# Optimization experiments

Measured on AMD Instinct MI355X. Metric: run time of the kernel, lower is better.

The kernel has to match this reference:

```python
import jax, jax.numpy as jnp
import numpy as np


def _conv1x1(w, b, x):
    # 1x1 Conv2d == channel matmul: w [O,C], x [B,C,H,W] -> [B,O,H,W]
    return jnp.einsum('oc,bchw->bohw', w, x) + b[None, :, None, None]


def setup_inputs() -> dict:
    key = jax.random.key(0)
    ks = jax.random.split(key, 9)
    C = 512
    B, H, W = 8, 32, 32
    s = 0.02
    return {
        'x': jax.random.normal(ks[0], (B, C, H, W), dtype=jnp.float32),
        'wq': jax.random.normal(ks[1], (C, C), dtype=jnp.float32) * s,
        'bq': jax.random.normal(ks[2], (C,), dtype=jnp.float32) * s,
        'wk': jax.random.normal(ks[3], (C, C), dtype=jnp.float32) * s,
        'bk': jax.random.normal(ks[4], (C,), dtype=jnp.float32) * s,
        'wv': jax.random.normal(ks[5], (C, C), dtype=jnp.float32) * s,
        'bv': jax.random.normal(ks[6], (C,), dtype=jnp.float32) * s,
        'wo': jax.random.normal(ks[7], (C, C), dtype=jnp.float32) * s,
        'bo': jax.random.normal(ks[8], (C,), dtype=jnp.float32) * s,
        'heads': 8,
    }


def reference(x, wq, bq, wk, bk, wv, bv, wo, bo, heads):
    B, C, H, W = x.shape
    N = H * W
    d = C // heads
    scale = jnp.asarray(d, x.dtype) ** 0.5

    vx = _conv1x1(wv, bv, x)                       # value(x), reused for residual
    Q = _conv1x1(wq, bq, x).reshape(B, heads, d, N)
    K = _conv1x1(wk, bk, x).reshape(B, heads, d, N)
    V = vx.reshape(B, heads, d, N)

    attn = jax.nn.softmax(jnp.einsum('bhcn,bhcm->bhnm', Q, K) / scale, axis=-1)
    attn_out = jnp.einsum('bhnm,bhcm->bhcn', attn, V).reshape(B, C, H, W)

    out = attn_out + vx                            # residual uses value(x)
    return _conv1x1(wo, bo, out)
```

## Files before the change

kernel.cpp:

```cpp
#include <hip/hip_runtime.h>
#include <cstdint>
#include <cmath>

#define B_ 8
#define C_ 512
#define N_ 1024
#define H_ 8
#define D_ 64


using u16 = unsigned short;

typedef __bf16 bf16x8 __attribute__((ext_vector_type(8)));
typedef float  f32x4  __attribute__((ext_vector_type(4)));
typedef unsigned short us8 __attribute__((ext_vector_type(8)));

#if __has_builtin(__builtin_amdgcn_exp2f)
#define EXP2(x) __builtin_amdgcn_exp2f(x)
#else
#define EXP2(x) exp2f(x)
#endif

#define QSCALE 0.1803368801111244f


__device__ __forceinline__ float b2f(u16 u) {
    return __uint_as_float(((uint32_t)u) << 16);
}
__device__ __forceinline__ u16 f2b(float f) {
    uint32_t x = __float_as_uint(f);
    return (u16)((x + 0x7fffu + ((x >> 16) & 1u)) >> 16);
}
__device__ __forceinline__ u16 f2bt(float f) {
    return (u16)(__float_as_uint(f) >> 16);
}
__device__ __forceinline__ float sf(float f) {
    return (fabsf(f) < 1e30f) ? f : 0.0f;
}
__device__ __forceinline__ u16 sf2b(float f) { return f2b(sf(f)); }

template<bool WB>
__device__ __forceinline__ us8 ldw(const void* W, size_t idx) {
    if constexpr (WB) {
        return *(const us8*)((const u16*)W + idx);
    } else {
        const float* p = (const float*)W + idx;
        float4 a = *(const float4*)p, b = *(const float4*)(p + 4);
        us8 pk;
        pk[0] = sf2b(a.x); pk[1] = sf2b(a.y); pk[2] = sf2b(a.z); pk[3] = sf2b(a.w);
        pk[4] = sf2b(b.x); pk[5] = sf2b(b.y); pk[6] = sf2b(b.z); pk[7] = sf2b(b.w);
        return pk;
    }
}


__global__ __launch_bounds__(256) void k_pre(const float* __restrict__ x,
                                             u16* __restrict__ xt,
                                             const float* __restrict__ wq,
                                             const float* __restrict__ wk,
                                             const float* __restrict__ wv,
                                             const float* __restrict__ wo,
                                             u16* __restrict__ wb) {
    const int tid = threadIdx.x;
    const int nb = blockIdx.x, cb = blockIdx.y, b = blockIdx.z;
    if (b == 8) {
        if (wb == nullptr) return;
        int base = (cb * 16 + nb) * 256 + tid;
#pragma unroll
        for (int i = 0; i < 8; ++i) {
            int idx = base + i * 32768;
            int m = idx >> 16;
            int off = (idx & 65535) << 2;
            const float* src = (m == 0) ? wq : (m == 1) ? wk : (m == 2) ? wv : wo;
            float4 v = *(const float4*)&src[off];
            ushort4 w;
            w.x = sf2b(v.x); w.y = sf2b(v.y); w.z = sf2b(v.z); w.w = sf2b(v.w);
            *(ushort4*)&wb[(m << 18) + off] = w;
        }
        return;
    }
    __shared__ __align__(16) u16 t[64][72];
#pragma unroll
    for (int i = 0; i < 4; ++i) {
        int q = tid + i * 256;
        int row = q >> 4, cg = q & 15;
        float4 v = *(const float4*)&x[((size_t)(b * C_ + cb * 64 + row) << 10) + nb * 64 + cg * 4];
        ushort4 w;
        w.x = sf2b(v.x); w.y = sf2b(v.y); w.z = sf2b(v.z); w.w = sf2b(v.w);
        *(ushort4*)&t[row][cg * 4] = w;
    }
    __syncthreads();
#pragma unroll
    for (int i = 0; i < 4; ++i) {
        int q = tid + i * 256;
        int nrow = q >> 4, cg = q & 15;
        ushort4 w;
        w.x = t[cg * 4 + 0][nrow];
        w.y = t[cg * 4 + 1][nrow];
        w.z = t[cg * 4 + 2][nrow];
        w.w = t[cg * 4 + 3][nrow];
        *(ushort4*)&xt[((size_t)(b * N_ + nb * 64 + nrow) << 9) + cb * 64 + cg * 4] = w;
    }
}


template<bool WB>
__global__ __launch_bounds__(256) void k_proj_t(
    const u16* __restrict__ xt,
    const void* __restrict__ wq, const float* __restrict__ bq,
    const void* __restrict__ wk, const float* __restrict__ bk,
    const void* __restrict__ wv, const float* __restrict__ bv,
    u16* __restrict__ qt, u16* __restrict__ kt,
    u16* __restrict__ v,  u16* __restrict__ vxt) {
    __shared__ __align__(16) u16 lA[128 * 64];
    __shared__ __align__(16) u16 lB[128 * 64];
    const int tid = threadIdx.x;
    const int op = blockIdx.z >> 3, b = blockIdx.z & 7;
    const int n0 = blockIdx.x * 128, o0 = blockIdx.y * 128;
    const void*  W  = (op == 0) ? wq : (op == 1) ? wk : wv;
    const float* BI = (op == 0) ? bq : (op == 1) ? bk : bv;
    const u16* A = xt + ((size_t)b << 19);
    const int lane = tid & 63, wave = tid >> 6;
    const int wm = (wave >> 1) * 64, wn = (wave & 1) * 64;
    const int l15 = lane & 15, lg = lane >> 4;
    const int xs = (l15 & 7) << 3;

    f32x4 acc[4][4];
    const f32x4 vzero = {0.f, 0.f, 0.f, 0.f};
#pragma unroll
    for (int i = 0; i < 4; ++i)
#pragma unroll
        for (int j = 0; j < 4; ++j) acc[i][j] = vzero;

    us8 ra[4], rwB[4];
    auto loadk = [&](int k0) {
#pragma unroll
        for (int p = 0; p < 4; ++p) {
            int slot = p * 256 + tid;
            int row = slot >> 3, seg = slot & 7;
            ra[p] = *(const us8*)&A[(size_t)(n0 + row) * C_ + k0 + seg * 8];
            rwB[p] = ldw<WB>(W, (size_t)(o0 + row) * C_ + k0 + seg * 8);
        }
    };
    loadk(0);

    for (int k0 = 0; k0 < C_; k0 += 64) {
        __syncthreads();
#pragma unroll
        for (int p = 0; p < 4; ++p) {
            int slot = p * 256 + tid;
            int row = slot >> 3, seg = slot & 7;
            int off = row * 64 + ((seg ^ (row & 7)) << 3);
            *(us8*)&lA[off] = ra[p];
            *(us8*)&lB[off] = rwB[p];
        }
        if (k0 + 64 < C_) loadk(k0 + 64);
        __syncthreads();
#pragma unroll
        for (int kk = 0; kk < 64; kk += 32) {
            const int col = (kk + lg * 8) ^ xs;
            bf16x8 af[4], bfr[4];
#pragma unroll
            for (int i = 0; i < 4; ++i)
                af[i] = *(const bf16x8*)&lA[(wm + i * 16 + l15) * 64 + col];
#pragma unroll
            for (int j = 0; j < 4; ++j)
                bfr[j] = *(const bf16x8*)&lB[(wn + j * 16 + l15) * 64 + col];
#pragma unroll
            for (int i = 0; i < 4; ++i)
#pragma unroll
                for (int j = 0; j < 4; ++j)
                    acc[i][j] = __builtin_amdgcn_mfma_f32_16x16x32_bf16(af[i], bfr[j], acc[i][j], 0, 0, 0);
        }
    }

    if (op < 2) {
        u16* outp = (op == 0) ? qt : kt;
        const float scl = (op == 0) ? QSCALE : 1.0f;
#pragma unroll
        for (int i = 0; i < 4; ++i) {
            int nb2 = n0 + wm + i * 16 + lg * 4;
#pragma unroll
            for (int j = 0; j < 4; ++j) {
                int o = o0 + wn + j * 16 + l15;
                float bias = sf(BI[o]);
                int h = o >> 6, dl = o & 63;
                size_t base = ((size_t)b * H_ + h) << 10;
#pragma unroll
                for (int r = 0; r < 4; ++r)
                    outp[(base + nb2 + r) * D_ + dl] = f2b((acc[i][j][r] + bias) * scl);
            }
        }
    } else {
#pragma unroll
        for (int i = 0; i < 4; ++i) {
            int nb2 = n0 + wm + i * 16 + lg * 4;
#pragma unroll
            for (int j = 0; j < 4; ++j) {
                int o = o0 + wn + j * 16 + l15;
                float bias = sf(BI[o]);
                float p0 = acc[i][j][0] + bias, p1 = acc[i][j][1] + bias;
                float p2 = acc[i][j][2] + bias, p3 = acc[i][j][3] + bias;
                ushort4 pk; pk.x = f2b(p0); pk.y = f2b(p1); pk.z = f2b(p2); pk.w = f2b(p3);
                *(ushort4*)&v[((size_t)(b * C_ + o) << 10) + nb2] = pk;
                vxt[((size_t)(b * N_ + nb2 + 0) << 9) + o] = pk.x;
                vxt[((size_t)(b * N_ + nb2 + 1) << 9) + o] = pk.y;
                vxt[((size_t)(b * N_ + nb2 + 2) << 9) + o] = pk.z;
                vxt[((size_t)(b * N_ + nb2 + 3) << 9) + o] = pk.w;
            }
        }
    }
}


__global__ __launch_bounds__(128, 2) void k_attn(
    const u16* __restrict__ qt, const u16* __restrict__ kt,
    const u16* __restrict__ v,  const u16* __restrict__ vxt,
    u16* __restrict__ rt) {
    __shared__ __align__(16) u16 lK[64 * 64];
    __shared__ __align__(16) u16 lV[64 * 64];
    __shared__ __align__(16) u16 lP[2][64 * 64];
    const int tid = threadIdx.x, lane = tid & 63, wave = tid >> 6;
    const int l15 = lane & 15, lg = lane >> 4;
    const int xs = (l15 & 7) << 3;
    const int bid = blockIdx.x;
    const int qb = bid >> 6, bh = bid & 63;
    const int b = bh >> 3, h = bh & 7;
    const size_t bh_off = (size_t)bh << 16;
    const int q0 = qb * 128;
    const int nA = wave * 64;

    bf16x8 qf[4][2];
#pragma unroll
    for (int nt = 0; nt < 4; ++nt)
#pragma unroll
        for (int k = 0; k < 2; ++k)
            qf[nt][k] = *(const bf16x8*)&qt[bh_off +
                (size_t)(q0 + nA + nt * 16 + l15) * D_ + k * 32 + lg * 8];

    us8 rk[4], rv[4];
    auto loadkv = [&](int mb) {
#pragma unroll
        for (int p = 0; p < 4; ++p) {
            int slot = p * 128 + tid;
            int row = slot >> 3, seg = slot & 7;
            rk[p] = *(const us8*)&kt[bh_off + (size_t)(mb * 64 + row) * D_ + seg * 8];
            rv[p] = *(const us8*)&v[((size_t)(b * C_ + h * 64 + row) << 10) + mb * 64 + seg * 8];
        }
    };
    loadkv(0);

    float L[4] = {0.f, 0.f, 0.f, 0.f};
    f32x4 oacc[4][4];
    const f32x4 vzero = {0.f, 0.f, 0.f, 0.f};
#pragma unroll
    for (int nt = 0; nt < 4; ++nt)
#pragma unroll
        for (int ct = 0; ct < 4; ++ct) oacc[nt][ct] = vzero;

    for (int mb = 0; mb < 16; ++mb) {
        __syncthreads();
#pragma unroll
        for (int p = 0; p < 4; ++p) {
            int slot = p * 128 + tid;
            int row = slot >> 3, seg = slot & 7;
            int off = row * 64 + ((seg ^ (row & 7)) << 3);
            *(us8*)&lK[off] = rk[p];
            *(us8*)&lV[off] = rv[p];
        }
        if (mb < 15) loadkv(mb + 1);
        __syncthreads();

        f32x4 s[4][4];
#pragma unroll
        for (int mt = 0; mt < 4; ++mt)
#pragma unroll
            for (int nt = 0; nt < 4; ++nt) s[mt][nt] = vzero;
#pragma unroll
        for (int k = 0; k < 2; ++k) {
            const int col = (k * 32 + lg * 8) ^ xs;
            bf16x8 aK[4];
#pragma unroll
            for (int mt = 0; mt < 4; ++mt)
                aK[mt] = *(const bf16x8*)&lK[(mt * 16 + l15) * 64 + col];
            __builtin_amdgcn_s_setprio(1);
#pragma unroll
            for (int mt = 0; mt < 4; ++mt)
#pragma unroll
                for (int nt = 0; nt < 4; ++nt)
                    s[mt][nt] = __builtin_amdgcn_mfma_f32_16x16x32_bf16(aK[mt], qf[nt][k], s[mt][nt], 0, 0, 0);
            __builtin_amdgcn_s_setprio(0);
        }

#pragma unroll
        for (int mt = 0; mt < 4; ++mt)
#pragma unroll
            for (int nt = 0; nt < 4; ++nt) {
                float p0 = EXP2(s[mt][nt][0]);
                float p1 = EXP2(s[mt][nt][1]);
                float p2 = EXP2(s[mt][nt][2]);
                float p3 = EXP2(s[mt][nt][3]);
                L[nt] += p0 + p1 + p2 + p3;
                ushort4 pk; pk.x = f2bt(p0); pk.y = f2bt(p1); pk.z = f2bt(p2); pk.w = f2bt(p3);
                *(ushort4*)&lP[wave][(nt * 16 + l15) * 64 + ((mt * 16 + lg * 4) ^ xs)] = pk;
            }

#pragma unroll
        for (int kk2 = 0; kk2 < 64; kk2 += 32) {
            const int colv = (kk2 + lg * 8) ^ xs;
            bf16x8 aP[4], bV[4];
#pragma unroll
            for (int nt = 0; nt < 4; ++nt)
                aP[nt] = *(const bf16x8*)&lP[wave][(nt * 16 + l15) * 64 + colv];
#pragma unroll
            for (int ct = 0; ct < 4; ++ct)
                bV[ct] = *(const bf16x8*)&lV[(ct * 16 + l15) * 64 + colv];
            __builtin_amdgcn_s_setprio(1);
#pragma unroll
            for (int nt = 0; nt < 4; ++nt)
#pragma unroll
                for (int ct = 0; ct < 4; ++ct)
                    oacc[nt][ct] = __builtin_amdgcn_mfma_f32_16x16x32_bf16(aP[nt], bV[ct], oacc[nt][ct], 0, 0, 0);
            __builtin_amdgcn_s_setprio(0);
        }
    }

#pragma unroll
    for (int nt = 0; nt < 4; ++nt) {
        float s2 = L[nt];
        s2 += __shfl_xor(s2, 16);
        s2 += __shfl_xor(s2, 32);
        L[nt] = s2;
    }

#pragma unroll
    for (int nt = 0; nt < 4; ++nt) {
        float inv[4];
#pragma unroll
        for (int r = 0; r < 4; ++r) inv[r] = 1.0f / __shfl(L[nt], lg * 4 + r);
#pragma unroll
        for (int ct = 0; ct < 4; ++ct) {
            int ch = h * 64 + ct * 16 + l15;
#pragma unroll
            for (int r = 0; r < 4; ++r) {
                int n = q0 + nA + nt * 16 + lg * 4 + r;
                size_t idx = ((size_t)(b * N_ + n) << 9) + ch;
                rt[idx] = f2b(oacc[nt][ct][r] * inv[r] + b2f(vxt[idx]));
            }
        }
    }
}


template<bool WB>
__global__ __launch_bounds__(256) void k_out_t(
    const u16* __restrict__ rt, const void* __restrict__ wo,
    const float* __restrict__ bo, float* __restrict__ out) {
    __shared__ __align__(16) u16 lA[128 * 64];
    __shared__ __align__(16) u16 lB[128 * 64];
    const int tid = threadIdx.x;
    const int b = blockIdx.z;
    const int n0 = blockIdx.x * 128, o0 = blockIdx.y * 128;
    const u16* Rb = rt + ((size_t)b << 19);
    const int lane = tid & 63, wave = tid >> 6;
    const int wm = (wave >> 1) * 64, wn = (wave & 1) * 64;
    const int l15 = lane & 15, lg = lane >> 4;
    const int xs = (l15 & 7) << 3;

    f32x4 acc[4][4];
    const f32x4 vzero = {0.f, 0.f, 0.f, 0.f};
#pragma unroll
    for (int i = 0; i < 4; ++i)
#pragma unroll
        for (int j = 0; j < 4; ++j) acc[i][j] = vzero;

    us8 rb[4], rwB[4];
    auto loadk = [&](int k0) {
#pragma unroll
        for (int p = 0; p < 4; ++p) {
            int slot = p * 256 + tid;
            int row = slot >> 3, seg = slot & 7;
            rwB[p] = ldw<WB>(wo, (size_t)(o0 + row) * C_ + k0 + seg * 8);
            rb[p] = *(const us8*)&Rb[(size_t)(n0 + row) * C_ + k0 + seg * 8];
        }
    };
    loadk(0);

    for (int k0 = 0; k0 < C_; k0 += 64) {
        __syncthreads();
#pragma unroll
        for (int p = 0; p < 4; ++p) {
            int slot = p * 256 + tid;
            int row = slot >> 3, seg = slot & 7;
            int off = row * 64 + ((seg ^ (row & 7)) << 3);
            *(us8*)&lA[off] = rwB[p];
            *(us8*)&lB[off] = rb[p];
        }
        if (k0 + 64 < C_) loadk(k0 + 64);
        __syncthreads();
#pragma unroll
        for (int kk = 0; kk < 64; kk += 32) {
            const int col = (kk + lg * 8) ^ xs;
            bf16x8 af[4], bfr[4];
#pragma unroll
            for (int i = 0; i < 4; ++i)
                af[i] = *(const bf16x8*)&lA[(wm + i * 16 + l15) * 64 + col];
#pragma unroll
            for (int j = 0; j < 4; ++j)
                bfr[j] = *(const bf16x8*)&lB[(wn + j * 16 + l15) * 64 + col];
#pragma unroll
            for (int i = 0; i < 4; ++i)
#pragma unroll
                for (int j = 0; j < 4; ++j)
                    acc[i][j] = __builtin_amdgcn_mfma_f32_16x16x32_bf16(af[i], bfr[j], acc[i][j], 0, 0, 0);
        }
    }

#pragma unroll
    for (int i = 0; i < 4; ++i) {
#pragma unroll
        for (int j = 0; j < 4; ++j) {
            int nn = n0 + wn + j * 16 + l15;
#pragma unroll
            for (int r = 0; r < 4; ++r) {
                int o = o0 + wm + i * 16 + lg * 4 + r;
                out[((size_t)(b * C_ + o) << 10) + nn] = acc[i][j][r] + sf(bo[o]);
            }
        }
    }
}


extern "C" void kernel_launch(void* const* d_in, const int* in_sizes, int n_in,
                              void* d_out, int out_size, void* d_ws, size_t ws_size,
                              hipStream_t stream) {
    const float* x  = (const float*)d_in[0];
    const float* wq = (const float*)d_in[1];
    const float* bq = (const float*)d_in[2];
    const float* wk = (const float*)d_in[3];
    const float* bk = (const float*)d_in[4];
    const float* wv = (const float*)d_in[5];
    const float* bv = (const float*)d_in[6];
    const float* wo = (const float*)d_in[7];
    const float* bo = (const float*)d_in[8];
    float* out = (float*)d_out;
    u16* ws = (u16*)d_ws;

    const size_t T = (size_t)B_ * C_ * N_;
    const size_t WSZ = (size_t)4 * C_ * C_;
    if (ws_size < 5 * T * sizeof(u16)) return;

    u16* xt  = ws;
    u16* qt  = ws + 1 * T;
    u16* kt  = ws + 2 * T;
    u16* vv  = ws + 3 * T;
    u16* vxt = ws + 4 * T;
    u16* rt  = xt;
    u16* wb  = ws + 5 * T;

    const bool wbfit = ws_size >= (5 * T + WSZ) * sizeof(u16);

    k_pre<<<dim3(16, 8, 9), 256, 0, stream>>>(x, xt, wq, wk, wv, wo,
                                              wbfit ? wb : (u16*)nullptr);
    if (wbfit) {
        k_proj_t<true><<<dim3(8, 4, 24), 256, 0, stream>>>(
            xt, wb, bq, wb + 262144, bk, wb + 524288, bv, qt, kt, vv, vxt);
    } else {
        k_proj_t<false><<<dim3(8, 4, 24), 256, 0, stream>>>(
            xt, wq, bq, wk, bk, wv, bv, qt, kt, vv, vxt);
    }
    k_attn<<<dim3(512), 128, 0, stream>>>(qt, kt, vv, vxt, rt);
    if (wbfit) {
        k_out_t<true><<<dim3(8, 4, 8), 256, 0, stream>>>(rt, wb + 786432, bo, out);
    } else {
        k_out_t<false><<<dim3(8, 4, 8), 256, 0, stream>>>(rt, wo, bo, out);
    }
}
```

Baseline: 93.19 us.

## Split attention KV range across two wave groups and merge partial results

The attention kernel now launches 256 threads per block. Two wave groups each process half of the key/value sequence for the same 128 query rows, and the partial outputs and row sums are combined through shared memory at the end. This is meant to shorten the serial KV loop per block and add waves to hide latency with the same 512-block grid. In exchange it doubles LDS use per block, which may limit occupancy, and it adds a shared-memory reduction step and extra barriers.

```diff
diff --git a/kernel.cpp b/kernel.cpp
--- a/kernel.cpp
+++ b/kernel.cpp
@@ -213,13 +213,14 @@
 }
 
 
-__global__ __launch_bounds__(128, 2) void k_attn(
+__global__ __launch_bounds__(256, 2) void k_attn(
     const u16* __restrict__ qt, const u16* __restrict__ kt,
     const u16* __restrict__ v,  const u16* __restrict__ vxt,
     u16* __restrict__ rt) {
-    __shared__ __align__(16) u16 lK[64 * 64];
-    __shared__ __align__(16) u16 lV[64 * 64];
-    __shared__ __align__(16) u16 lP[2][64 * 64];
+    __shared__ __align__(16) u16 lK[2][64 * 64];
+    __shared__ __align__(16) u16 lV[2][64 * 64];
+    __shared__ __align__(16) u16 lP[4][64 * 64];
+    __shared__ float lL[2][64];
     const int tid = threadIdx.x, lane = tid & 63, wave = tid >> 6;
     const int l15 = lane & 15, lg = lane >> 4;
     const int xs = (l15 & 7) << 3;
@@ -228,7 +229,10 @@
     const int b = bh >> 3, h = bh & 7;
     const size_t bh_off = (size_t)bh << 16;
     const int q0 = qb * 128;
-    const int nA = wave * 64;
+    const int kvh = wave >> 1;
+    const int qh = wave & 1;
+    const int nA = qh * 64;
+    const int ht = tid & 127;
 
     bf16x8 qf[4][2];
 #pragma unroll
@@ -239,10 +243,11 @@
                 (size_t)(q0 + nA + nt * 16 + l15) * D_ + k * 32 + lg * 8];
 
     us8 rk[4], rv[4];
-    auto loadkv = [&](int mb) {
+    auto loadkv = [&](int it) {
+        int mb = kvh * 8 + it;
 #pragma unroll
         for (int p = 0; p < 4; ++p) {
-            int slot = p * 128 + tid;
+            int slot = p * 128 + ht;
             int row = slot >> 3, seg = slot & 7;
             rk[p] = *(const us8*)&kt[bh_off + (size_t)(mb * 64 + row) * D_ + seg * 8];
             rv[p] = *(const us8*)&v[((size_t)(b * C_ + h * 64 + row) << 10) + mb * 64 + seg * 8];
@@ -258,17 +263,17 @@
 #pragma unroll
         for (int ct = 0; ct < 4; ++ct) oacc[nt][ct] = vzero;
 
-    for (int mb = 0; mb < 16; ++mb) {
+    for (int it = 0; it < 8; ++it) {
         __syncthreads();
 #pragma unroll
         for (int p = 0; p < 4; ++p) {
-            int slot = p * 128 + tid;
+            int slot = p * 128 + ht;
             int row = slot >> 3, seg = slot & 7;
             int off = row * 64 + ((seg ^ (row & 7)) << 3);
-            *(us8*)&lK[off] = rk[p];
-            *(us8*)&lV[off] = rv[p];
-        }
-        if (mb < 15) loadkv(mb + 1);
+            *(us8*)&lK[kvh][off] = rk[p];
+            *(us8*)&lV[kvh][off] = rv[p];
+        }
+        if (it < 7) loadkv(it + 1);
         __syncthreads();
 
         f32x4 s[4][4];
@@ -282,7 +287,7 @@
             bf16x8 aK[4];
 #pragma unroll
             for (int mt = 0; mt < 4; ++mt)
-                aK[mt] = *(const bf16x8*)&lK[(mt * 16 + l15) * 64 + col];
+                aK[mt] = *(const bf16x8*)&lK[kvh][(mt * 16 + l15) * 64 + col];
             __builtin_amdgcn_s_setprio(1);
 #pragma unroll
             for (int mt = 0; mt < 4; ++mt)
@@ -314,7 +319,7 @@
                 aP[nt] = *(const bf16x8*)&lP[wave][(nt * 16 + l15) * 64 + colv];
 #pragma unroll
             for (int ct = 0; ct < 4; ++ct)
-                bV[ct] = *(const bf16x8*)&lV[(ct * 16 + l15) * 64 + colv];
+                bV[ct] = *(const bf16x8*)&lV[kvh][(ct * 16 + l15) * 64 + colv];
             __builtin_amdgcn_s_setprio(1);
 #pragma unroll
             for (int nt = 0; nt < 4; ++nt)
@@ -331,6 +336,40 @@
         s2 += __shfl_xor(s2, 16);
         s2 += __shfl_xor(s2, 32);
         L[nt] = s2;
+    }
+
+    __syncthreads();
+    float* fO = (float*)&lP[0][0];
+    if (kvh == 1) {
+#pragma unroll
+        for (int nt = 0; nt < 4; ++nt) {
+            if (lg == 0) lL[qh][nt * 16 + l15] = L[nt];
+#pragma unroll
+            for (int ct = 0; ct < 4; ++ct) {
+#pragma unroll
+                for (int r = 0; r < 4; ++r) {
+                    int n = nt * 16 + lg * 4 + r;
+                    int c = (ct * 16 + l15) ^ (((n >> 2) & 1) << 4);
+                    fO[qh * 4096 + n * 64 + c] = oacc[nt][ct][r];
+                }
+            }
+        }
+    }
+    __syncthreads();
+    if (kvh == 1) return;
+
+#pragma unroll
+    for (int nt = 0; nt < 4; ++nt) {
+        L[nt] += lL[qh][nt * 16 + l15];
+#pragma unroll
+        for (int ct = 0; ct < 4; ++ct) {
+#pragma unroll
+            for (int r = 0; r < 4; ++r) {
+                int n = nt * 16 + lg * 4 + r;
+                int c = (ct * 16 + l15) ^ (((n >> 2) & 1) << 4);
+                oacc[nt][ct][r] += fO[qh * 4096 + n * 64 + c];
+            }
+        }
     }
 
 #pragma unroll
@@ -469,7 +508,7 @@
         k_proj_t<false><<<dim3(8, 4, 24), 256, 0, stream>>>(
             xt, wq, bq, wk, bk, wv, bv, qt, kt, vv, vxt);
     }
-    k_attn<<<dim3(512), 128, 0, stream>>>(qt, kt, vv, vxt, rt);
+    k_attn<<<dim3(512), 256, 0, stream>>>(qt, kt, vv, vxt, rt);
     if (wbfit) {
         k_out_t<true><<<dim3(8, 4, 8), 256, 0, stream>>>(rt, wb + 786432, bo, out);
     } else {
```

After: 75.74 us, median of 2. -18.7%, faster.
